# Kernel optimization log

Measured on AMD Instinct MI355X. Metric: run time of the kernel, lower is better.

## Reference

```python
import jax, jax.numpy as jnp
import numpy as np

B, T, D_IN, H, D_OUT = 64, 512, 512, 1024, 512

def _uniform(key, shape, bound):
    return jax.random.uniform(key, shape, jnp.float32, -bound, bound)

def setup_inputs() -> dict:
    key = jax.random.key(0)
    ks = jax.random.split(key, 12)
    bnd = 1.0 / np.sqrt(H)  # PyTorch nn.RNN / nn.Linear init bound
    return {
        "x": jax.random.normal(ks[0], (B, T, D_IN), jnp.float32),
        "W_ih0": _uniform(ks[1], (H, D_IN), bnd),
        "W_hh0": _uniform(ks[2], (H, H), bnd),
        "b_ih0": _uniform(ks[3], (H,), bnd),
        "b_hh0": _uniform(ks[4], (H,), bnd),
        "W_ih1": _uniform(ks[5], (H, H), bnd),
        "W_hh1": _uniform(ks[6], (H, H), bnd),
        "b_ih1": _uniform(ks[7], (H,), bnd),
        "b_hh1": _uniform(ks[8], (H,), bnd),
        "W_fc": _uniform(ks[9], (D_OUT, H), bnd),
        "b_fc": _uniform(ks[10], (D_OUT,), bnd),
    }

def _rnn_layer(seq, W_ih, W_hh, b_ih, b_hh):
    # seq: [B, T, D]; tanh vanilla RNN, h0 = 0 (as in the torch forward)
    pre = jnp.einsum('btd,hd->bth', seq, W_ih) + b_ih  # input GEMM batched over time
    h0 = jnp.zeros((seq.shape[0], W_hh.shape[0]), seq.dtype)
    def step(h, p):
        h = jnp.tanh(p + h @ W_hh.T + b_hh)
        return h, h
    _, hs = jax.lax.scan(step, h0, jnp.swapaxes(pre, 0, 1))  # [T, B, H]
    return jnp.swapaxes(hs, 0, 1)  # [B, T, H]

def reference(x, W_ih0, W_hh0, b_ih0, b_hh0, W_ih1, W_hh1, b_ih1, b_hh1, W_fc, b_fc):
    h1 = _rnn_layer(x, W_ih0, W_hh0, b_ih0, b_hh0)
    h2 = _rnn_layer(h1, W_ih1, W_hh1, b_ih1, b_hh1)
    last = h2[:, -1, :]  # only the final timestep feeds the head
    return last @ W_fc.T + b_fc
```

## Files before the change

### kernel.cpp

```cpp
#include <hip/hip_runtime.h>
#include <stdint.h>

#define BB   64
#define TT   512
#define DIN  512
#define HH   1024
#define DOUT 512

#define GROUPS        4
#define ROWS          16
#define WGS_PER_GROUP 16
#define NSLICE        64
#define THREADS       512
#define NW            8
#define PSTR          18
#define PBUF          (NW * 4 * 16 * PSTR)
#define SSTR          36
#define SENT          0x7fff7fffu

typedef __attribute__((ext_vector_type(8))) short frag8;
typedef __attribute__((ext_vector_type(4))) float f32x4;
typedef __attribute__((ext_vector_type(4))) unsigned int u32x4;

union U4F8 { u32x4 u; frag8 f; };

__device__ __forceinline__ float bf2f(unsigned short u) {
  union { unsigned int i; float f; } v; v.i = ((unsigned int)u) << 16; return v.f;
}
__device__ __forceinline__ unsigned short f2bf(float f) {
  union { float f; unsigned int i; } v; v.f = f;
  unsigned int x = v.i;
  x += 0x7fffu + ((x >> 16) & 1u);
  return (unsigned short)(x >> 16);
}
__device__ __forceinline__ frag8 ld8f32(const float* p) {
  frag8 r;
#pragma unroll
  for (int j = 0; j < 8; ++j) r[j] = (short)f2bf(p[j]);
  return r;
}

__device__ __forceinline__ bool ldx4_poll(frag8 a[4], const unsigned short* p) {
  u32x4 t0, t1, t2, t3;
  asm volatile(
      "global_load_dwordx4 %0, %4, off sc1\n\t"
      "global_load_dwordx4 %1, %4, off offset:64 sc1\n\t"
      "global_load_dwordx4 %2, %4, off offset:128 sc1\n\t"
      "global_load_dwordx4 %3, %4, off offset:192 sc1\n\t"
      "s_waitcnt vmcnt(0)"
      : "=&v"(t0), "=&v"(t1), "=&v"(t2), "=&v"(t3)
      : "v"(p)
      : "memory");
  bool ok = (t0[0] != SENT) & (t0[1] != SENT) & (t0[2] != SENT) & (t0[3] != SENT)
          & (t1[0] != SENT) & (t1[1] != SENT) & (t1[2] != SENT) & (t1[3] != SENT)
          & (t2[0] != SENT) & (t2[1] != SENT) & (t2[2] != SENT) & (t2[3] != SENT)
          & (t3[0] != SENT) & (t3[1] != SENT) & (t3[2] != SENT) & (t3[3] != SENT);
  U4F8 u;
  u.u = t0; a[0] = u.f;  u.u = t1; a[1] = u.f;
  u.u = t2; a[2] = u.f;  u.u = t3; a[3] = u.f;
  return __ballot(ok) == ~0ull;
}
__device__ __forceinline__ void poll256(frag8 a[4], const unsigned short* p) {
  if (ldx4_poll(a, p)) return;
  for (;;) {
    __builtin_amdgcn_s_sleep(12);
    if (ldx4_poll(a, p)) return;
  }
}
__device__ __forceinline__ void st128_sc1(unsigned int* p, u32x4 v) {
  asm volatile("global_store_dwordx4 %0, %1, off sc1" :: "v"(p), "v"(v) : "memory");
}

template<int KIN, bool L0>
__device__ void scan_body(const void* Xv,
                          const float* Wih, const float* Whh,
                          const float* bih, const float* bhh,
                          unsigned short* S,
                          int g, int s, float* parts, unsigned int* stage)
{
  constexpr int KIT_IN = KIN / (NW * 32);
  constexpr int KIT_HH = HH  / (NW * 32);

  const int j0  = s * NSLICE;
  const int r0  = g * ROWS;
  const int tid = threadIdx.x;
  const int w   = tid >> 6;
  const int l   = tid & 63;
  const int lm  = l & 15;
  const int lq  = l >> 4;

  frag8 wih_f[KIT_IN][4];
  frag8 whh_f[KIT_HH][4];
#pragma unroll
  for (int kit = 0; kit < KIT_IN; ++kit)
#pragma unroll
    for (int nt = 0; nt < 4; ++nt) {
      int n = j0 + nt * 16 + lm;
      int k = w * (KIN / NW) + kit * 32 + lq * 8;
      wih_f[kit][nt] = ld8f32(Wih + (size_t)n * KIN + k);
    }
#pragma unroll
  for (int kit = 0; kit < KIT_HH; ++kit)
#pragma unroll
    for (int nt = 0; nt < 4; ++nt) {
      int n = j0 + nt * 16 + lm;
      int k = w * (HH / NW) + kit * 32 + lq * 8;
      whh_f[kit][nt] = ld8f32(Whh + (size_t)n * HH + k);
    }

  const int erow = tid & 15;
  const int ecg  = tid >> 4;
  float bias2[2];
#pragma unroll
  for (int j = 0; j < 2; ++j) {
    int c = j0 + ecg * 2 + j;
    bias2[j] = bih[c] + bhh[c];
  }
  const int prow = tid >> 3;
  const int pc8  = tid & 7;

  const size_t koff = (size_t)w * (KIN / NW) + (size_t)lq * 8;

  float4 xa[2 * KIT_IN];
  frag8  xf[KIT_IN];
  if constexpr (L0) {
    const float* xr = (const float*)Xv + ((size_t)(r0 + lm) * TT + 0) * KIN + koff;
#pragma unroll
    for (int kit = 0; kit < KIT_IN; ++kit) {
      xa[2 * kit]     = *(const float4*)(xr + kit * 32);
      xa[2 * kit + 1] = *(const float4*)(xr + kit * 32 + 4);
    }
  } else {
    const unsigned short* px = (const unsigned short*)Xv
        + ((size_t)(r0 + lm) * TT + 0) * KIN + koff;
    poll256(xf, px);
  }

  for (int t = 0; t < TT; ++t) {
    f32x4 acc[4];
#pragma unroll
    for (int nt = 0; nt < 4; ++nt) acc[nt] = (f32x4){0.f, 0.f, 0.f, 0.f};

    if constexpr (L0) {
#pragma unroll
      for (int kit = 0; kit < KIT_IN; ++kit) {
        const float* f0 = (const float*)&xa[2 * kit];
        const float* f1 = (const float*)&xa[2 * kit + 1];
        frag8 a;
#pragma unroll
        for (int j = 0; j < 4; ++j) {
          a[j]     = (short)f2bf(f0[j]);
          a[4 + j] = (short)f2bf(f1[j]);
        }
#pragma unroll
        for (int nt = 0; nt < 4; ++nt)
          acc[nt] = __builtin_amdgcn_mfma_f32_16x16x32_bf16(a, wih_f[kit][nt], acc[nt], 0, 0, 0);
      }
      if (t + 1 < TT) {
        const float* xr = (const float*)Xv
            + ((size_t)(r0 + lm) * TT + (t + 1)) * KIN + koff;
#pragma unroll
        for (int kit = 0; kit < KIT_IN; ++kit) {
          xa[2 * kit]     = *(const float4*)(xr + kit * 32);
          xa[2 * kit + 1] = *(const float4*)(xr + kit * 32 + 4);
        }
      }
    } else {
#pragma unroll
      for (int kit = 0; kit < KIT_IN; ++kit)
#pragma unroll
        for (int nt = 0; nt < 4; ++nt)
          acc[nt] = __builtin_amdgcn_mfma_f32_16x16x32_bf16(xf[kit], wih_f[kit][nt], acc[nt], 0, 0, 0);
    }

    if (t > 0) {
      const unsigned short* ph = S + ((size_t)(r0 + lm) * TT + (t - 1)) * HH
                                   + (size_t)w * (HH / NW) + lq * 8;
      frag8 hf[KIT_HH];
      poll256(hf, ph);
#pragma unroll
      for (int kit = 0; kit < KIT_HH; ++kit)
#pragma unroll
        for (int nt = 0; nt < 4; ++nt)
          acc[nt] = __builtin_amdgcn_mfma_f32_16x16x32_bf16(hf[kit], whh_f[kit][nt], acc[nt], 0, 0, 0);
    }

    float* pb = parts + (t & 1) * PBUF;
#pragma unroll
    for (int nt = 0; nt < 4; ++nt)
#pragma unroll
      for (int r = 0; r < 4; ++r)
        pb[((w * 4 + nt) * 16 + lq * 4 + r) * PSTR + lm] = acc[nt][r];
    __syncthreads();

    unsigned int hb2 = 0;
#pragma unroll
    for (int j = 0; j < 2; ++j) {
      int c  = ecg * 2 + j;
      int nt = c >> 4;
      int lc = c & 15;
      float sm = 0.f;
#pragma unroll
      for (int w8 = 0; w8 < NW; ++w8)
        sm += pb[((w8 * 4 + nt) * 16 + erow) * PSTR + lc];
      float u = sm + bias2[j];
      float e = __expf(2.0f * u);
      float hv = 1.0f - 2.0f / (e + 1.0f);
      hb2 |= (unsigned int)f2bf(hv) << (16 * j);
    }
    stage[erow * SSTR + ecg] = hb2;
    __syncthreads();

    if (tid < 128) {
      u32x4 v = *(const u32x4*)(stage + prow * SSTR + pc8 * 4);
      unsigned short* dst = S + ((size_t)(r0 + prow) * TT + t) * HH + j0 + pc8 * 8;
      st128_sc1((unsigned int*)dst, v);
    }

    if constexpr (!L0) {
      if (t + 1 < TT) {
        const unsigned short* px = (const unsigned short*)Xv
            + ((size_t)(r0 + lm) * TT + (t + 1)) * KIN + koff;
        poll256(xf, px);
      }
    }
  }
}

__global__ __launch_bounds__(THREADS, 1)
void rnn_fused(const float* x,
               const float* Wih0, const float* Whh0, const float* bih0, const float* bhh0,
               const float* Wih1, const float* Whh1, const float* bih1, const float* bhh1,
               unsigned short* h1seq, unsigned short* h2seq)
{
  __shared__ float parts[2 * PBUF];
  __shared__ unsigned int stage[16 * SSTR];
  const int wg = blockIdx.x;
  if (wg < GROUPS * WGS_PER_GROUP) {
    const int g = wg / WGS_PER_GROUP, s = wg % WGS_PER_GROUP;
    scan_body<DIN, true>(x, Wih0, Whh0, bih0, bhh0, h1seq, g, s, parts, stage);
  } else {
    const int wg2 = wg - GROUPS * WGS_PER_GROUP;
    const int g = wg2 / WGS_PER_GROUP, s = wg2 % WGS_PER_GROUP;
    scan_body<HH, false>(h1seq, Wih1, Whh1, bih1, bhh1, h2seq, g, s, parts, stage);
  }
}

__global__ void poison_kernel(uint4* __restrict__ p, int n4) {
  int i  = blockIdx.x * blockDim.x + threadIdx.x;
  int st = gridDim.x * blockDim.x;
  const uint4 v = make_uint4(SENT, SENT, SENT, SENT);
  for (; i < n4; i += st) p[i] = v;
}

__global__ void fc_kernel(const unsigned short* __restrict__ h2seq,
                          const float* __restrict__ Wfc,
                          const float* __restrict__ bfc,
                          float* __restrict__ out)
{
  int idx = blockIdx.x * blockDim.x + threadIdx.x;
  int m = idx >> 9;
  int n = idx & 511;
  const unsigned short* hp = h2seq + ((size_t)m * TT + (TT - 1)) * HH;
  const float*          wp = Wfc + (size_t)n * HH;
  float acc = 0.f;
#pragma unroll 4
  for (int k = 0; k < HH; k += 4) {
    ushort4 hv = *(const ushort4*)(hp + k);
    float4  wv = *(const float4*)(wp + k);
    acc += bf2f(hv.x) * wv.x + bf2f(hv.y) * wv.y
         + bf2f(hv.z) * wv.z + bf2f(hv.w) * wv.w;
  }
  out[idx] = acc + bfc[n];
}

extern "C" void kernel_launch(void* const* d_in, const int* in_sizes, int n_in,
                              void* d_out, int out_size, void* d_ws, size_t ws_size,
                              hipStream_t stream)
{
  const float* x    = (const float*)d_in[0];
  const float* Wih0 = (const float*)d_in[1];
  const float* Whh0 = (const float*)d_in[2];
  const float* bih0 = (const float*)d_in[3];
  const float* bhh0 = (const float*)d_in[4];
  const float* Wih1 = (const float*)d_in[5];
  const float* Whh1 = (const float*)d_in[6];
  const float* bih1 = (const float*)d_in[7];
  const float* bhh1 = (const float*)d_in[8];
  const float* Wfc  = (const float*)d_in[9];
  const float* bfc  = (const float*)d_in[10];

  unsigned char* ws = (unsigned char*)d_ws;
  unsigned short* h1seq = (unsigned short*)ws;
  unsigned short* h2seq = (unsigned short*)(ws + (size_t)BB * TT * HH * 2);

  poison_kernel<<<4096, 256, 0, stream>>>(
      (uint4*)ws, (int)(((size_t)BB * TT * HH * 2 * 2) / 16));

  rnn_fused<<<2 * GROUPS * WGS_PER_GROUP, THREADS, 0, stream>>>(
      x, Wih0, Whh0, bih0, bhh0, Wih1, Whh1, bih1, bhh1, h1seq, h2seq);

  fc_kernel<<<(BB * DOUT) / 256, 256, 0, stream>>>(h2seq, Wfc, bfc, (float*)d_out);
}
```

Before: 1.827 ms.

## Replace sentinel-poisoned data polling with per-timestep ready flags

Instead of poisoning the whole 128MB h1/h2 workspace with sentinel values and spinning on the data itself, each producer wave now drains its store and sets a per-timestep flag word. Consumers spin on a 16-byte flag vector and then do plain loads of the hidden state. The Whh MFMA work is also moved ahead of the next x prefetch in layer 0. This removes the large poison memset and the sentinel checks, but adds a store-drain plus extra flag store and flag load on the per-step critical path, and it relies on plain loads seeing data after the flag.

Measured after the change: 2.299 ms. 1.26x slower.

```diff
diff --git a/kernel.cpp b/kernel.cpp
--- a/kernel.cpp
+++ b/kernel.cpp
@@ -16,13 +16,12 @@
 #define PSTR          18
 #define PBUF          (NW * 4 * 16 * PSTR)
 #define SSTR          36
-#define SENT          0x7fff7fffu
+#define FL_PER_T      32
+#define FLWORDS       (2 * GROUPS * TT * FL_PER_T)
 
 typedef __attribute__((ext_vector_type(8))) short frag8;
 typedef __attribute__((ext_vector_type(4))) float f32x4;
 typedef __attribute__((ext_vector_type(4))) unsigned int u32x4;
-
-union U4F8 { u32x4 u; frag8 f; };
 
 __device__ __forceinline__ float bf2f(unsigned short u) {
   union { unsigned int i; float f; } v; v.i = ((unsigned int)u) << 16; return v.f;
@@ -40,35 +39,28 @@
   return r;
 }
 
-__device__ __forceinline__ bool ldx4_poll(frag8 a[4], const unsigned short* p) {
-  u32x4 t0, t1, t2, t3;
-  asm volatile(
-      "global_load_dwordx4 %0, %4, off sc1\n\t"
-      "global_load_dwordx4 %1, %4, off offset:64 sc1\n\t"
-      "global_load_dwordx4 %2, %4, off offset:128 sc1\n\t"
-      "global_load_dwordx4 %3, %4, off offset:192 sc1\n\t"
-      "s_waitcnt vmcnt(0)"
-      : "=&v"(t0), "=&v"(t1), "=&v"(t2), "=&v"(t3)
-      : "v"(p)
-      : "memory");
-  bool ok = (t0[0] != SENT) & (t0[1] != SENT) & (t0[2] != SENT) & (t0[3] != SENT)
-          & (t1[0] != SENT) & (t1[1] != SENT) & (t1[2] != SENT) & (t1[3] != SENT)
-          & (t2[0] != SENT) & (t2[1] != SENT) & (t2[2] != SENT) & (t2[3] != SENT)
-          & (t3[0] != SENT) & (t3[1] != SENT) & (t3[2] != SENT) & (t3[3] != SENT);
-  U4F8 u;
-  u.u = t0; a[0] = u.f;  u.u = t1; a[1] = u.f;
-  u.u = t2; a[2] = u.f;  u.u = t3; a[3] = u.f;
-  return __ballot(ok) == ~0ull;
-}
-__device__ __forceinline__ void poll256(frag8 a[4], const unsigned short* p) {
-  if (ldx4_poll(a, p)) return;
+__device__ __forceinline__ void flag_spin4(const unsigned int* fp) {
   for (;;) {
-    __builtin_amdgcn_s_sleep(12);
-    if (ldx4_poll(a, p)) return;
-  }
+    u32x4 f;
+    asm volatile(
+        "global_load_dwordx4 %0, %1, off sc1\n\t"
+        "s_waitcnt vmcnt(0)"
+        : "=&v"(f) : "v"(fp) : "memory");
+    if ((f[0] & f[1] & f[2] & f[3]) != 0u) break;
+  }
+}
+__device__ __forceinline__ void ld4_plain(frag8 a[4], const unsigned short* p) {
+  const frag8* q = (const frag8*)p;
+  a[0] = q[0]; a[1] = q[4]; a[2] = q[8]; a[3] = q[12];
+}
+__device__ __forceinline__ void st32_sc1(unsigned int* p, unsigned int v) {
+  asm volatile("global_store_dword %0, %1, off sc1" :: "v"(p), "v"(v) : "memory");
 }
 __device__ __forceinline__ void st128_sc1(unsigned int* p, u32x4 v) {
   asm volatile("global_store_dwordx4 %0, %1, off sc1" :: "v"(p), "v"(v) : "memory");
+}
+__device__ __forceinline__ void drain_vm() {
+  asm volatile("s_waitcnt vmcnt(0)" ::: "memory");
 }
 
 template<int KIN, bool L0>
@@ -76,6 +68,7 @@
                           const float* Wih, const float* Whh,
                           const float* bih, const float* bhh,
                           unsigned short* S,
+                          unsigned int* flS, const unsigned int* flX,
                           int g, int s, float* parts, unsigned int* stage)
 {
   constexpr int KIT_IN = KIN / (NW * 32);
@@ -120,6 +113,7 @@
   const int pc8  = tid & 7;
 
   const size_t koff = (size_t)w * (KIN / NW) + (size_t)lq * 8;
+  const int fcw = 4 * w;
 
   float4 xa[2 * KIT_IN];
   frag8  xf[KIT_IN];
@@ -131,9 +125,9 @@
       xa[2 * kit + 1] = *(const float4*)(xr + kit * 32 + 4);
     }
   } else {
-    const unsigned short* px = (const unsigned short*)Xv
-        + ((size_t)(r0 + lm) * TT + 0) * KIN + koff;
-    poll256(xf, px);
+    flag_spin4(flX + 0 * FL_PER_T + fcw);
+    ld4_plain(xf, (const unsigned short*)Xv
+                      + ((size_t)(r0 + lm) * TT + 0) * KIN + koff);
   }
 
   for (int t = 0; t < TT; ++t) {
@@ -156,6 +150,27 @@
         for (int nt = 0; nt < 4; ++nt)
           acc[nt] = __builtin_amdgcn_mfma_f32_16x16x32_bf16(a, wih_f[kit][nt], acc[nt], 0, 0, 0);
       }
+    } else {
+#pragma unroll
+      for (int kit = 0; kit < KIT_IN; ++kit)
+#pragma unroll
+        for (int nt = 0; nt < 4; ++nt)
+          acc[nt] = __builtin_amdgcn_mfma_f32_16x16x32_bf16(xf[kit], wih_f[kit][nt], acc[nt], 0, 0, 0);
+    }
+
+    if (t > 0) {
+      flag_spin4(flS + (t - 1) * FL_PER_T + fcw);
+      frag8 hf[KIT_HH];
+      ld4_plain(hf, S + ((size_t)(r0 + lm) * TT + (t - 1)) * HH
+                        + (size_t)w * (HH / NW) + lq * 8);
+#pragma unroll
+      for (int kit = 0; kit < KIT_HH; ++kit)
+#pragma unroll
+        for (int nt = 0; nt < 4; ++nt)
+          acc[nt] = __builtin_amdgcn_mfma_f32_16x16x32_bf16(hf[kit], whh_f[kit][nt], acc[nt], 0, 0, 0);
+    }
+
+    if constexpr (L0) {
       if (t + 1 < TT) {
         const float* xr = (const float*)Xv
             + ((size_t)(r0 + lm) * TT + (t + 1)) * KIN + koff;
@@ -165,24 +180,6 @@
           xa[2 * kit + 1] = *(const float4*)(xr + kit * 32 + 4);
         }
       }
-    } else {
-#pragma unroll
-      for (int kit = 0; kit < KIT_IN; ++kit)
-#pragma unroll
-        for (int nt = 0; nt < 4; ++nt)
-          acc[nt] = __builtin_amdgcn_mfma_f32_16x16x32_bf16(xf[kit], wih_f[kit][nt], acc[nt], 0, 0, 0);
-    }
-
-    if (t > 0) {
-      const unsigned short* ph = S + ((size_t)(r0 + lm) * TT + (t - 1)) * HH
-                                   + (size_t)w * (HH / NW) + lq * 8;
-      frag8 hf[KIT_HH];
-      poll256(hf, ph);
-#pragma unroll
-      for (int kit = 0; kit < KIT_HH; ++kit)
-#pragma unroll
-        for (int nt = 0; nt < 4; ++nt)
-          acc[nt] = __builtin_amdgcn_mfma_f32_16x16x32_bf16(hf[kit], whh_f[kit][nt], acc[nt], 0, 0, 0);
     }
 
     float* pb = parts + (t & 1) * PBUF;
@@ -215,13 +212,16 @@
       u32x4 v = *(const u32x4*)(stage + prow * SSTR + pc8 * 4);
       unsigned short* dst = S + ((size_t)(r0 + prow) * TT + t) * HH + j0 + pc8 * 8;
       st128_sc1((unsigned int*)dst, v);
+      drain_vm();
+      if (l == 0)
+        st32_sc1(flS + t * FL_PER_T + s * 2 + (tid >> 6), 1u);
     }
 
     if constexpr (!L0) {
       if (t + 1 < TT) {
-        const unsigned short* px = (const unsigned short*)Xv
-            + ((size_t)(r0 + lm) * TT + (t + 1)) * KIN + koff;
-        poll256(xf, px);
+        flag_spin4(flX + (t + 1) * FL_PER_T + fcw);
+        ld4_plain(xf, (const unsigned short*)Xv
+                          + ((size_t)(r0 + lm) * TT + (t + 1)) * KIN + koff);
       }
     }
   }
@@ -231,26 +231,30 @@
 void rnn_fused(const float* x,
                const float* Wih0, const float* Whh0, const float* bih0, const float* bhh0,
                const float* Wih1, const float* Whh1, const float* bih1, const float* bhh1,
-               unsigned short* h1seq, unsigned short* h2seq)
+               unsigned short* h1seq, unsigned short* h2seq, unsigned int* flags)
 {
   __shared__ float parts[2 * PBUF];
   __shared__ unsigned int stage[16 * SSTR];
   const int wg = blockIdx.x;
   if (wg < GROUPS * WGS_PER_GROUP) {
     const int g = wg / WGS_PER_GROUP, s = wg % WGS_PER_GROUP;
-    scan_body<DIN, true>(x, Wih0, Whh0, bih0, bhh0, h1seq, g, s, parts, stage);
+    unsigned int* fl0g = flags + (size_t)g * TT * FL_PER_T;
+    scan_body<DIN, true>(x, Wih0, Whh0, bih0, bhh0, h1seq,
+                         fl0g, nullptr, g, s, parts, stage);
   } else {
     const int wg2 = wg - GROUPS * WGS_PER_GROUP;
     const int g = wg2 / WGS_PER_GROUP, s = wg2 % WGS_PER_GROUP;
-    scan_body<HH, false>(h1seq, Wih1, Whh1, bih1, bhh1, h2seq, g, s, parts, stage);
-  }
-}
-
-__global__ void poison_kernel(uint4* __restrict__ p, int n4) {
+    unsigned int* fl0g = flags + (size_t)g * TT * FL_PER_T;
+    unsigned int* fl1g = flags + (size_t)(GROUPS + g) * TT * FL_PER_T;
+    scan_body<HH, false>(h1seq, Wih1, Whh1, bih1, bhh1, h2seq,
+                         fl1g, fl0g, g, s, parts, stage);
+  }
+}
+
+__global__ void zero_kernel(unsigned int* __restrict__ p, int n) {
   int i  = blockIdx.x * blockDim.x + threadIdx.x;
   int st = gridDim.x * blockDim.x;
-  const uint4 v = make_uint4(SENT, SENT, SENT, SENT);
-  for (; i < n4; i += st) p[i] = v;
+  for (; i < n; i += st) p[i] = 0u;
 }
 
 __global__ void fc_kernel(const unsigned short* __restrict__ h2seq,
@@ -293,12 +297,12 @@
   unsigned char* ws = (unsigned char*)d_ws;
   unsigned short* h1seq = (unsigned short*)ws;
   unsigned short* h2seq = (unsigned short*)(ws + (size_t)BB * TT * HH * 2);
-
-  poison_kernel<<<4096, 256, 0, stream>>>(
-      (uint4*)ws, (int)(((size_t)BB * TT * HH * 2 * 2) / 16));
+  unsigned int*   flags = (unsigned int*)(ws + 2 * (size_t)BB * TT * HH * 2);
+
+  zero_kernel<<<64, 256, 0, stream>>>(flags, FLWORDS);
 
   rnn_fused<<<2 * GROUPS * WGS_PER_GROUP, THREADS, 0, stream>>>(
-      x, Wih0, Whh0, bih0, bhh0, Wih1, Whh1, bih1, bhh1, h1seq, h2seq);
+      x, Wih0, Whh0, bih0, bhh0, Wih1, Whh1, bih1, bhh1, h1seq, h2seq, flags);
 
   fc_kernel<<<(BB * DOUT) / 256, 256, 0, stream>>>(h2seq, Wfc, bfc, (float*)d_out);
 }
```
